# Optimization experiments

Hardware: AMD Instinct MI355X
Metric: run time of the kernel (lower is better)

The kernel has to match this reference:

```python
import jax, jax.numpy as jnp
import numpy as np

INPUT_DIM = 2048
HIDDEN_DIM = 256  # max(input_dim // 8, 32)
NUM_EXPERTS = 16
TOP_K = 2
Z_LOSS_COEF = 0.005
LB_COEF = 0.005
LN_EPS = 1e-5


def setup_inputs() -> dict:
    key = jax.random.key(0)
    k1, k2, k3 = jax.random.split(key, 3)
    B, S = 4, 4096
    x = jax.random.normal(k1, (B, S, INPUT_DIM), dtype=jnp.float32)
    # orthogonal-ish init approximated by scaled gaussian (math is identical regardless of values)
    Wp = jax.random.normal(k2, (HIDDEN_DIM, INPUT_DIM), dtype=jnp.float32) * (0.3 / np.sqrt(INPUT_DIM))
    Wg = jax.random.normal(k3, (NUM_EXPERTS, HIDDEN_DIM), dtype=jnp.float32) * (0.3 / np.sqrt(HIDDEN_DIM))
    ln_w = jnp.ones((HIDDEN_DIM,), dtype=jnp.float32)
    ln_b = jnp.zeros((HIDDEN_DIM,), dtype=jnp.float32)
    temperature = jnp.ones((1,), dtype=jnp.float32) * 0.07
    return {"x": x, "Wp": Wp, "Wg": Wg, "ln_w": ln_w, "ln_b": ln_b, "temperature": temperature}


def reference(x, Wp, Wg, ln_w, ln_b, temperature):
    B, S, D = x.shape
    xr = x.reshape(-1, D)                                  # [T, D]
    proj = jnp.einsum('td,hd->th', xr, Wp)                 # [T, H]
    mu = proj.mean(-1, keepdims=True)
    var = jnp.mean(jnp.square(proj - mu), axis=-1, keepdims=True)
    normalized = (proj - mu) * jax.lax.rsqrt(var + LN_EPS) * ln_w + ln_b
    logits = jnp.einsum('th,eh->te', normalized, Wg)       # [T, E]
    # temperature used via .item() in torch -> constant w.r.t. autodiff
    temp = jax.lax.stop_gradient(jnp.abs(temperature) + 1e-6)[0]
    logits = logits / temp
    routing_weights = jax.nn.softmax(logits, axis=-1)      # [T, E]
    top_k_w, top_k_i = jax.lax.top_k(routing_weights, TOP_K)
    top_k_w = top_k_w / (top_k_w.sum(-1, keepdims=True) + 1e-6)
    T = routing_weights.shape[0]
    dispatch = jnp.zeros_like(routing_weights).at[jnp.arange(T)[:, None], top_k_i].set(top_k_w)
    # load-balance KL: F.kl_div(actual.log(), ideal, reduction='batchmean')
    E = routing_weights.shape[-1]
    actual_load = routing_weights.mean(0)                  # [E]
    ideal = 1.0 / E
    load_balance_loss = jnp.sum(ideal * (jnp.log(ideal) - jnp.log(actual_load))) / E
    router_z_loss = jnp.mean(jnp.square(logits))
    router_loss = Z_LOSS_COEF * router_z_loss + LB_COEF * load_balance_loss
    return (jax.lax.stop_gradient(routing_weights), dispatch.reshape(B, S, E), router_loss)
```

## Files before the change

### kernel.cpp

```cpp
#include <hip/hip_runtime.h>
#include <hip/hip_bf16.h>
#include <math.h>

#define D 2048
#define H 256
#define E 16
#define TMB 64
#define BK 16
#define NCH (D / BK)
#define LDK 20
#define WP_OFF 0
#define X_OFF 5120
#define SB_LDW 257
#define SB_OFF 0
#define WG_OFF 8224
#define LB_OFF 12320
#define Z_OFF  12336
#define SMEM_FLOATS 12352
#define THREADS 1024
#define WS_STRIDE 20

__global__ __launch_bounds__(THREADS, 4)
void router_main(const float* __restrict__ x, const float* __restrict__ Wp,
                 const float* __restrict__ Wg, const float* __restrict__ lnw_g,
                 const float* __restrict__ lnb_g, const float* __restrict__ temp_g,
                 float* __restrict__ out_rw, float* __restrict__ out_disp,
                 float* __restrict__ ws_part)
{
    __shared__ __align__(16) float smem[SMEM_FLOATS];
    const int t  = threadIdx.x;
    const int tx = t & 15;
    const int ku = (t >> 4) & 3;
    const int wv = t >> 6;
    const int tb = wv & 7;
    const int hb = wv >> 3;
    const int wrow = t >> 2;
    const int wcol = (t & 3) << 2;
    const int tok0 = blockIdx.x * TMB;

    *(float4*)&smem[WG_OFF + 4 * t] = *(const float4*)&Wg[4 * t];

    float acc[8][8];
    #pragma unroll
    for (int i = 0; i < 8; ++i)
        #pragma unroll
        for (int j = 0; j < 8; ++j) acc[i][j] = 0.f;

    float4 wpr, xr;
    auto ISSUE = [&](int k0) {
        wpr = *(const float4*)&Wp[(size_t)wrow * D + k0 + wcol];
        if (t < 256) xr = *(const float4*)&x[(size_t)(tok0 + wrow) * D + k0 + wcol];
    };
    ISSUE(0);

    const float* wbase = &smem[WP_OFF + (hb * 128 + tx) * LDK + ku * 4];
    const float* xbase = &smem[X_OFF + tb * 128 + ku * 4];

    for (int c = 0; c < NCH; ++c) {
        __syncthreads();
        *(float4*)&smem[WP_OFF + wrow * LDK + wcol] = wpr;
        if (t < 256) *(float4*)&smem[X_OFF + wrow * 16 + wcol] = xr;
        __syncthreads();
        if (c + 1 < NCH) ISSUE((c + 1) * BK);

        float4 xa[8];
        #pragma unroll
        for (int i = 0; i < 8; ++i)
            xa[i] = *(const float4*)&xbase[i * 16];
        #pragma unroll
        for (int j = 0; j < 8; ++j) {
            const float4 wvv = *(const float4*)&wbase[j * 16 * LDK];
            #pragma unroll
            for (int i = 0; i < 8; ++i) {
                acc[i][j] = fmaf(xa[i].x, wvv.x, acc[i][j]);
                acc[i][j] = fmaf(xa[i].y, wvv.y, acc[i][j]);
                acc[i][j] = fmaf(xa[i].z, wvv.z, acc[i][j]);
                acc[i][j] = fmaf(xa[i].w, wvv.w, acc[i][j]);
            }
        }
    }

    #pragma unroll
    for (int i = 0; i < 8; ++i)
        #pragma unroll
        for (int j = 0; j < 8; ++j) {
            acc[i][j] += __shfl_xor(acc[i][j], 16);
            acc[i][j] += __shfl_xor(acc[i][j], 32);
        }

    __syncthreads();

    const float temp = fabsf(temp_g[0]) + 1e-6f;
    float lnw[16], lnb[16];
    if (t < 512) {
        #pragma unroll
        for (int j = 0; j < 16; ++j) {
            lnw[j] = lnw_g[(t & 15) + 16 * j];
            lnb[j] = lnb_g[(t & 15) + 16 * j];
        }
    }
    float mylb = 0.f, myz = 0.f;

    #pragma unroll
    for (int pass = 0; pass < 2; ++pass) {
        if (ku == 0 && (tb >> 2) == pass) {
            const int rb = (tb & 3) * 8;
            #pragma unroll
            for (int i = 0; i < 8; ++i)
                #pragma unroll
                for (int j = 0; j < 8; ++j)
                    smem[SB_OFF + (rb + i) * SB_LDW + hb * 128 + tx + 16 * j] = acc[i][j];
        }
        if (pass == 0) {
            if (t < 16)  smem[LB_OFF + t] = 0.f;
            if (t == 16) smem[Z_OFF] = 0.f;
        }
        __syncthreads();

        if (t < 512) {
            const int ptx  = t & 15;
            const int tokl = t >> 4;
            const int tok  = tok0 + pass * 32 + tokl;

            float pr[16];
            #pragma unroll
            for (int j = 0; j < 16; ++j)
                pr[j] = smem[SB_OFF + tokl * SB_LDW + ptx + 16 * j];

            float s = 0.f;
            #pragma unroll
            for (int j = 0; j < 16; ++j) s += pr[j];
            s += __shfl_xor(s, 1); s += __shfl_xor(s, 2);
            s += __shfl_xor(s, 4); s += __shfl_xor(s, 8);
            const float mu = s * (1.f / 256.f);
            float v = 0.f;
            #pragma unroll
            for (int j = 0; j < 16; ++j) { const float d = pr[j] - mu; v = fmaf(d, d, v); }
            v += __shfl_xor(v, 1); v += __shfl_xor(v, 2);
            v += __shfl_xor(v, 4); v += __shfl_xor(v, 8);
            const float rstd = 1.0f / sqrtf(v * (1.f / 256.f) + 1e-5f);

            float n[16];
            #pragma unroll
            for (int j = 0; j < 16; ++j)
                n[j] = fmaf((pr[j] - mu) * rstd, lnw[j], lnb[j]);

            float p[16];
            #pragma unroll
            for (int e = 0; e < 16; ++e) p[e] = 0.f;
            #pragma unroll
            for (int j = 0; j < 16; ++j) {
                const float nv = n[j];
                const int  h   = ptx + 16 * j;
                #pragma unroll
                for (int e = 0; e < 16; ++e)
                    p[e] = fmaf(nv, smem[WG_OFF + e * H + h], p[e]);
            }
            #pragma unroll
            for (int m = 1; m < 16; m <<= 1)
                #pragma unroll
                for (int e = 0; e < 16; ++e) p[e] += __shfl_xor(p[e], m);
            #pragma unroll
            for (int e = 0; e < 16; ++e) p[e] = p[e] / temp;

            if (ptx == 0) {
                #pragma unroll
                for (int e = 0; e < 16; ++e) myz = fmaf(p[e], p[e], myz);
            }

            float mx = p[0];
            #pragma unroll
            for (int e = 1; e < 16; ++e) mx = fmaxf(mx, p[e]);
            float w[16]; float sw = 0.f;
            #pragma unroll
            for (int e = 0; e < 16; ++e) { w[e] = expf(p[e] - mx); sw += w[e]; }
            #pragma unroll
            for (int e = 0; e < 16; ++e) w[e] = w[e] / sw;
            mylb += w[ptx];

            float w1 = -1.f; int i1 = 0; float w2 = -1.f; int i2 = 0;
            #pragma unroll
            for (int e = 0; e < 16; ++e) {
                const float we = w[e];
                if (we > w1)      { w2 = w1; i2 = i1; w1 = we; i1 = e; }
                else if (we > w2) { w2 = we; i2 = e; }
            }
            const float rs = 1.f / (w1 + w2 + 1e-6f);
            out_rw  [(size_t)tok * E + ptx] = w[ptx];
            out_disp[(size_t)tok * E + ptx] = (ptx == i1) ? w1 * rs : (ptx == i2 ? w2 * rs : 0.f);
        }
        __syncthreads();
    }

    if (t < 512) {
        mylb += __shfl_xor(mylb, 16); mylb += __shfl_xor(mylb, 32);
        myz  += __shfl_xor(myz, 16);  myz  += __shfl_xor(myz, 32);
        if ((t & 63) < 16) atomicAdd(&smem[LB_OFF + (t & 15)], mylb);
        if ((t & 63) == 0) atomicAdd(&smem[Z_OFF], myz);
    }
    __syncthreads();
    if (t < 16)  ws_part[blockIdx.x * WS_STRIDE + t]  = smem[LB_OFF + t];
    if (t == 16) ws_part[blockIdx.x * WS_STRIDE + 16] = smem[Z_OFF];
}

__global__ void router_final(const float* __restrict__ ws_part,
                             float* __restrict__ out_loss, int nblocks, int T)
{
    const int l = threadIdx.x;
    float lb[16]; float z = 0.f;
    #pragma unroll
    for (int e = 0; e < 16; ++e) lb[e] = 0.f;
    for (int b = l; b < nblocks; b += 64) {
        #pragma unroll
        for (int e = 0; e < 16; ++e) lb[e] += ws_part[b * WS_STRIDE + e];
        z += ws_part[b * WS_STRIDE + 16];
    }
    #pragma unroll
    for (int m = 1; m < 64; m <<= 1) {
        #pragma unroll
        for (int e = 0; e < 16; ++e) lb[e] += __shfl_xor(lb[e], m);
        z += __shfl_xor(z, m);
    }
    if (l == 0) {
        const float zloss = z / (float)(T * 16);
        const float ideal = 1.f / 16.f;
        float lbl = 0.f;
        #pragma unroll
        for (int e = 0; e < 16; ++e) {
            const float a = lb[e] / (float)T;
            lbl += ideal * (logf(ideal) - logf(a));
        }
        lbl *= (1.f / 16.f);
        out_loss[0] = 0.005f * zloss + 0.005f * lbl;
    }
}

extern "C" void kernel_launch(void* const* d_in, const int* in_sizes, int n_in,
                              void* d_out, int out_size, void* d_ws, size_t ws_size,
                              hipStream_t stream)
{
    const float* x    = (const float*)d_in[0];
    const float* Wp   = (const float*)d_in[1];
    const float* Wg   = (const float*)d_in[2];
    const float* lnw  = (const float*)d_in[3];
    const float* lnb  = (const float*)d_in[4];
    const float* temp = (const float*)d_in[5];
    const int T = in_sizes[0] / D;
    float* out      = (float*)d_out;
    float* out_rw   = out;
    float* out_disp = out + (size_t)T * E;
    float* out_loss = out + (size_t)2 * T * E;
    float* ws_part  = (float*)d_ws;
    const int nblocks = T / TMB;

    hipLaunchKernelGGL(router_main, dim3(nblocks), dim3(THREADS), 0, stream,
                       x, Wp, Wg, lnw, lnb, temp, out_rw, out_disp, ws_part);
    hipLaunchKernelGGL(router_final, dim3(1), dim3(64), 0, stream,
                       ws_part, out_loss, nblocks, T);
}
```

Measured before the change: 294.9 us.

## Shrink token tile to 16 with 256-thread blocks and single-pass epilogue

Reduces tokens per block from 64 to 16 and threads from 1024 to 256, so each thread loads four Wp rows per k-chunk. The LayerNorm/gating epilogue now runs in one pass instead of two. This creates four times as many blocks for better scheduling and occupancy. The cost is that each block re-streams the full Wp matrix, quadrupling Wp traffic and lowering reuse.

```diff
diff --git a/kernel.cpp b/kernel.cpp
--- a/kernel.cpp
+++ b/kernel.cpp
@@ -5,7 +5,7 @@
 #define D 2048
 #define H 256
 #define E 16
-#define TMB 64
+#define TMB 16
 #define BK 16
 #define NCH (D / BK)
 #define LDK 20
@@ -13,11 +13,11 @@
 #define X_OFF 5120
 #define SB_LDW 257
 #define SB_OFF 0
-#define WG_OFF 8224
-#define LB_OFF 12320
-#define Z_OFF  12336
-#define SMEM_FLOATS 12352
-#define THREADS 1024
+#define WG_OFF 5376
+#define LB_OFF 9472
+#define Z_OFF  9488
+#define SMEM_FLOATS 9504
+#define THREADS 256
 #define WS_STRIDE 20
 
 __global__ __launch_bounds__(THREADS, 4)
@@ -32,13 +32,15 @@
     const int tx = t & 15;
     const int ku = (t >> 4) & 3;
     const int wv = t >> 6;
-    const int tb = wv & 7;
-    const int hb = wv >> 3;
+    const int tb = wv & 1;
+    const int hb = wv >> 1;
     const int wrow = t >> 2;
     const int wcol = (t & 3) << 2;
     const int tok0 = blockIdx.x * TMB;
 
-    *(float4*)&smem[WG_OFF + 4 * t] = *(const float4*)&Wg[4 * t];
+    #pragma unroll
+    for (int p = 0; p < 4; ++p)
+        *(float4*)&smem[WG_OFF + (p * 256 + t) * 4] = *(const float4*)&Wg[(p * 256 + t) * 4];
 
     float acc[8][8];
     #pragma unroll
@@ -46,10 +48,12 @@
         #pragma unroll
         for (int j = 0; j < 8; ++j) acc[i][j] = 0.f;
 
-    float4 wpr, xr;
+    float4 wst[4], xst;
     auto ISSUE = [&](int k0) {
-        wpr = *(const float4*)&Wp[(size_t)wrow * D + k0 + wcol];
-        if (t < 256) xr = *(const float4*)&x[(size_t)(tok0 + wrow) * D + k0 + wcol];
+        #pragma unroll
+        for (int p = 0; p < 4; ++p)
+            wst[p] = *(const float4*)&Wp[(size_t)(p * 64 + wrow) * D + k0 + wcol];
+        if (t < 64) xst = *(const float4*)&x[(size_t)(tok0 + (t >> 2)) * D + k0 + wcol];
     };
     ISSUE(0);
 
@@ -58,8 +62,10 @@
 
     for (int c = 0; c < NCH; ++c) {
         __syncthreads();
-        *(float4*)&smem[WP_OFF + wrow * LDK + wcol] = wpr;
-        if (t < 256) *(float4*)&smem[X_OFF + wrow * 16 + wcol] = xr;
+        #pragma unroll
+        for (int p = 0; p < 4; ++p)
+            *(float4*)&smem[WP_OFF + (p * 64 + wrow) * LDK + wcol] = wst[p];
+        if (t < 64) *(float4*)&smem[X_OFF + (t >> 2) * 16 + wcol] = xst;
         __syncthreads();
         if (c + 1 < NCH) ISSUE((c + 1) * BK);
 
@@ -90,114 +96,101 @@
 
     __syncthreads();
 
+    if (ku == 0) {
+        #pragma unroll
+        for (int i = 0; i < 8; ++i)
+            #pragma unroll
+            for (int j = 0; j < 8; ++j)
+                smem[SB_OFF + (tb * 8 + i) * SB_LDW + hb * 128 + tx + 16 * j] = acc[i][j];
+    }
+    if (t < 16)  smem[LB_OFF + t] = 0.f;
+    if (t == 16) smem[Z_OFF] = 0.f;
+    __syncthreads();
+
+    const int ptx  = t & 15;
+    const int tokl = t >> 4;
+    const int tok  = tok0 + tokl;
     const float temp = fabsf(temp_g[0]) + 1e-6f;
+
     float lnw[16], lnb[16];
-    if (t < 512) {
-        #pragma unroll
-        for (int j = 0; j < 16; ++j) {
-            lnw[j] = lnw_g[(t & 15) + 16 * j];
-            lnb[j] = lnb_g[(t & 15) + 16 * j];
-        }
-    }
-    float mylb = 0.f, myz = 0.f;
-
-    #pragma unroll
-    for (int pass = 0; pass < 2; ++pass) {
-        if (ku == 0 && (tb >> 2) == pass) {
-            const int rb = (tb & 3) * 8;
-            #pragma unroll
-            for (int i = 0; i < 8; ++i)
-                #pragma unroll
-                for (int j = 0; j < 8; ++j)
-                    smem[SB_OFF + (rb + i) * SB_LDW + hb * 128 + tx + 16 * j] = acc[i][j];
-        }
-        if (pass == 0) {
-            if (t < 16)  smem[LB_OFF + t] = 0.f;
-            if (t == 16) smem[Z_OFF] = 0.f;
-        }
-        __syncthreads();
-
-        if (t < 512) {
-            const int ptx  = t & 15;
-            const int tokl = t >> 4;
-            const int tok  = tok0 + pass * 32 + tokl;
-
-            float pr[16];
-            #pragma unroll
-            for (int j = 0; j < 16; ++j)
-                pr[j] = smem[SB_OFF + tokl * SB_LDW + ptx + 16 * j];
-
-            float s = 0.f;
-            #pragma unroll
-            for (int j = 0; j < 16; ++j) s += pr[j];
-            s += __shfl_xor(s, 1); s += __shfl_xor(s, 2);
-            s += __shfl_xor(s, 4); s += __shfl_xor(s, 8);
-            const float mu = s * (1.f / 256.f);
-            float v = 0.f;
-            #pragma unroll
-            for (int j = 0; j < 16; ++j) { const float d = pr[j] - mu; v = fmaf(d, d, v); }
-            v += __shfl_xor(v, 1); v += __shfl_xor(v, 2);
-            v += __shfl_xor(v, 4); v += __shfl_xor(v, 8);
-            const float rstd = 1.0f / sqrtf(v * (1.f / 256.f) + 1e-5f);
-
-            float n[16];
-            #pragma unroll
-            for (int j = 0; j < 16; ++j)
-                n[j] = fmaf((pr[j] - mu) * rstd, lnw[j], lnb[j]);
-
-            float p[16];
-            #pragma unroll
-            for (int e = 0; e < 16; ++e) p[e] = 0.f;
-            #pragma unroll
-            for (int j = 0; j < 16; ++j) {
-                const float nv = n[j];
-                const int  h   = ptx + 16 * j;
-                #pragma unroll
-                for (int e = 0; e < 16; ++e)
-                    p[e] = fmaf(nv, smem[WG_OFF + e * H + h], p[e]);
-            }
-            #pragma unroll
-            for (int m = 1; m < 16; m <<= 1)
-                #pragma unroll
-                for (int e = 0; e < 16; ++e) p[e] += __shfl_xor(p[e], m);
-            #pragma unroll
-            for (int e = 0; e < 16; ++e) p[e] = p[e] / temp;
-
-            if (ptx == 0) {
-                #pragma unroll
-                for (int e = 0; e < 16; ++e) myz = fmaf(p[e], p[e], myz);
-            }
-
-            float mx = p[0];
-            #pragma unroll
-            for (int e = 1; e < 16; ++e) mx = fmaxf(mx, p[e]);
-            float w[16]; float sw = 0.f;
-            #pragma unroll
-            for (int e = 0; e < 16; ++e) { w[e] = expf(p[e] - mx); sw += w[e]; }
-            #pragma unroll
-            for (int e = 0; e < 16; ++e) w[e] = w[e] / sw;
-            mylb += w[ptx];
-
-            float w1 = -1.f; int i1 = 0; float w2 = -1.f; int i2 = 0;
-            #pragma unroll
-            for (int e = 0; e < 16; ++e) {
-                const float we = w[e];
-                if (we > w1)      { w2 = w1; i2 = i1; w1 = we; i1 = e; }
-                else if (we > w2) { w2 = we; i2 = e; }
-            }
-            const float rs = 1.f / (w1 + w2 + 1e-6f);
-            out_rw  [(size_t)tok * E + ptx] = w[ptx];
-            out_disp[(size_t)tok * E + ptx] = (ptx == i1) ? w1 * rs : (ptx == i2 ? w2 * rs : 0.f);
-        }
-        __syncthreads();
-    }
-
-    if (t < 512) {
-        mylb += __shfl_xor(mylb, 16); mylb += __shfl_xor(mylb, 32);
-        myz  += __shfl_xor(myz, 16);  myz  += __shfl_xor(myz, 32);
-        if ((t & 63) < 16) atomicAdd(&smem[LB_OFF + (t & 15)], mylb);
-        if ((t & 63) == 0) atomicAdd(&smem[Z_OFF], myz);
-    }
+    #pragma unroll
+    for (int j = 0; j < 16; ++j) {
+        lnw[j] = lnw_g[ptx + 16 * j];
+        lnb[j] = lnb_g[ptx + 16 * j];
+    }
+
+    float pr[16];
+    #pragma unroll
+    for (int j = 0; j < 16; ++j)
+        pr[j] = smem[SB_OFF + tokl * SB_LDW + ptx + 16 * j];
+
+    float s = 0.f;
+    #pragma unroll
+    for (int j = 0; j < 16; ++j) s += pr[j];
+    s += __shfl_xor(s, 1); s += __shfl_xor(s, 2);
+    s += __shfl_xor(s, 4); s += __shfl_xor(s, 8);
+    const float mu = s * (1.f / 256.f);
+    float v = 0.f;
+    #pragma unroll
+    for (int j = 0; j < 16; ++j) { const float d = pr[j] - mu; v = fmaf(d, d, v); }
+    v += __shfl_xor(v, 1); v += __shfl_xor(v, 2);
+    v += __shfl_xor(v, 4); v += __shfl_xor(v, 8);
+    const float rstd = 1.0f / sqrtf(v * (1.f / 256.f) + 1e-5f);
+
+    float n[16];
+    #pragma unroll
+    for (int j = 0; j < 16; ++j)
+        n[j] = fmaf((pr[j] - mu) * rstd, lnw[j], lnb[j]);
+
+    float p[16];
+    #pragma unroll
+    for (int e = 0; e < 16; ++e) p[e] = 0.f;
+    #pragma unroll
+    for (int j = 0; j < 16; ++j) {
+        const float nv = n[j];
+        const int  h   = ptx + 16 * j;
+        #pragma unroll
+        for (int e = 0; e < 16; ++e)
+            p[e] = fmaf(nv, smem[WG_OFF + e * H + h], p[e]);
+    }
+    #pragma unroll
+    for (int m = 1; m < 16; m <<= 1)
+        #pragma unroll
+        for (int e = 0; e < 16; ++e) p[e] += __shfl_xor(p[e], m);
+    #pragma unroll
+    for (int e = 0; e < 16; ++e) p[e] = p[e] / temp;
+
+    float myz = 0.f;
+    if (ptx == 0) {
+        #pragma unroll
+        for (int e = 0; e < 16; ++e) myz = fmaf(p[e], p[e], myz);
+    }
+
+    float mx = p[0];
+    #pragma unroll
+    for (int e = 1; e < 16; ++e) mx = fmaxf(mx, p[e]);
+    float w[16]; float sw = 0.f;
+    #pragma unroll
+    for (int e = 0; e < 16; ++e) { w[e] = expf(p[e] - mx); sw += w[e]; }
+    #pragma unroll
+    for (int e = 0; e < 16; ++e) w[e] = w[e] / sw;
+
+    float w1 = -1.f; int i1 = 0; float w2 = -1.f; int i2 = 0;
+    #pragma unroll
+    for (int e = 0; e < 16; ++e) {
+        const float we = w[e];
+        if (we > w1)      { w2 = w1; i2 = i1; w1 = we; i1 = e; }
+        else if (we > w2) { w2 = we; i2 = e; }
+    }
+    const float rs = 1.f / (w1 + w2 + 1e-6f);
+    out_rw  [(size_t)tok * E + ptx] = w[ptx];
+    out_disp[(size_t)tok * E + ptx] = (ptx == i1) ? w1 * rs : (ptx == i2 ? w2 * rs : 0.f);
+
+    float mylb = w[ptx];
+    mylb += __shfl_xor(mylb, 16); mylb += __shfl_xor(mylb, 32);
+    myz  += __shfl_xor(myz, 16);  myz  += __shfl_xor(myz, 32);
+    if ((t & 63) < 16) atomicAdd(&smem[LB_OFF + ptx], mylb);
+    if ((t & 63) == 0) atomicAdd(&smem[Z_OFF], myz);
     __syncthreads();
     if (t < 16)  ws_part[blockIdx.x * WS_STRIDE + t]  = smem[LB_OFF + t];
     if (t == 16) ws_part[blockIdx.x * WS_STRIDE + 16] = smem[Z_OFF];
```

New measurement: 645.1 us. +118.7%, slower.
